# Kernel tuning notes

Hardware: AMD Instinct MI355X
Metric: run time of the kernel (lower is better)

The kernel has to match this reference:

```python
import jax, jax.numpy as jnp
import numpy as np

A, B, N = 8, 8, 2048


def setup_inputs() -> dict:
    key = jax.random.key(0)
    k1, k2 = jax.random.split(key)
    p_src = jax.random.normal(k1, (A, B, N, 2), dtype=jnp.float32)
    p_dst = jax.random.normal(k2, (A, B, N, 2), dtype=jnp.float32)
    return {"p_src": p_src, "p_dst": p_dst, "height": 480, "width": 640, "grid_scale": 1}


def reference(p_src, p_dst, height, width, grid_scale):
    a_dim, b_dim, n_pts = p_src.shape[:3]
    grid_h, grid_w = int(height * grid_scale), int(width * grid_scale)
    M = a_dim * b_dim * n_pts  # static upper bound on #matches

    # denormalize_pixel_coordinates(p, grid_h, grid_w): (x,y) -> ((p+1) * [(gw-1)/2, (gh-1)/2])
    scale = jnp.array([(grid_w - 1) / 2.0, (grid_h - 1) / 2.0], dtype=jnp.float32)
    coord_src = (p_src + 1.0) * scale  # [A,B,N,2] float grid coords (x,y)
    coord_dst = (p_dst + 1.0) * scale

    vis_src = jnp.all((p_src >= -1) & (p_src <= 1), axis=-1)  # [A,B,N]
    vis_dst = jnp.all((p_dst >= -1) & (p_dst <= 1), axis=-1)

    # integer cell coords; route invisible points out of bounds so scatter drops them
    xs = jnp.where(vis_src, coord_src[..., 0].astype(jnp.int32), grid_w).reshape(-1)
    ys = jnp.where(vis_src, coord_src[..., 1].astype(jnp.int32), grid_h).reshape(-1)
    xd = jnp.where(vis_dst, coord_dst[..., 0].astype(jnp.int32), grid_w).reshape(-1)
    yd = jnp.where(vis_dst, coord_dst[..., 1].astype(jnp.int32), grid_h).reshape(-1)

    ids = jnp.arange(M, dtype=jnp.int32)  # flat point index == torch's compacted-order rank
    aa = jnp.broadcast_to(jnp.arange(a_dim, dtype=jnp.int32)[:, None, None], (a_dim, b_dim, n_pts)).reshape(-1)
    bb = jnp.broadcast_to(jnp.arange(b_dim, dtype=jnp.int32)[None, :, None], (a_dim, b_dim, n_pts)).reshape(-1)

    grid0 = jnp.full((a_dim, b_dim, grid_w, grid_h), -1, dtype=jnp.int32)
    grid0 = grid0.at[aa, bb, xs, ys].max(ids, mode='drop')
    grid1 = jnp.full((a_dim, b_dim, grid_w, grid_h), -1, dtype=jnp.int32)
    grid1 = grid1.at[aa, bb, xd, yd].max(ids, mode='drop')

    mask_f = ((grid0 >= 0) & (grid1 >= 0)).reshape(-1)
    sel = jnp.nonzero(mask_f, size=M, fill_value=0)[0]  # row-major == torch boolean-mask order
    valid = jnp.arange(M) < jnp.sum(mask_f)

    src_idx = grid0.reshape(-1)[sel]  # flat point index of matched src point
    dst_idx = grid1.reshape(-1)[sel]

    # NOTE: faithful to source: factor pairs (height-1)/(grid_h-1) with the x column
    factor = jnp.array([(height - 1) / (grid_h - 1), (width - 1) / (grid_w - 1)], dtype=jnp.float32)
    csf = (coord_src * factor).reshape(-1, 2)
    cdf = (coord_dst * factor).reshape(-1, 2)

    src_coord_m = jnp.where(valid[:, None], csf[src_idx], 0.0)  # [M,2], padded with 0
    dst_coord_m = jnp.where(valid[:, None], cdf[dst_idx], 0.0)
    # visible_src_idx[:, match][[1,2]].T -> (b, n); visible_dst_idx[:, match][[0,2]].T -> (a, n)
    src_bn = jnp.where(valid[:, None], jnp.stack([(src_idx // n_pts) % b_dim, src_idx % n_pts], axis=-1), -1)
    dst_an = jnp.where(valid[:, None], jnp.stack([dst_idx // (b_dim * n_pts), dst_idx % n_pts], axis=-1), -1)
    return src_coord_m, dst_coord_m, src_bn, dst_an, valid
```

## Files before the change

### kernel.cpp

```cpp
#include <hip/hip_runtime.h>

#define AD 8
#define BD 8
#define NP 2048
#define MPTS (AD*BD*NP)
#define NIMG (AD*BD)
#define NSPI 4
#define NSEG (NIMG*NSPI)
#define HSZ 4096
#define RCAP 2048
#define DPAD 65536

__device__ int g_cnt[NSEG];
__device__ int g_rc[NSEG*RCAP];
__device__ int g_rs[NSEG*RCAP];
__device__ int g_rd[NSEG*RCAP];

__global__ __launch_bounds__(256) void k_hash(
    const float* __restrict__ ps, const float* __restrict__ pd,
    float* __restrict__ out,
    const int* __restrict__ ph, const int* __restrict__ pw,
    const int* __restrict__ pg) {
  __shared__ int hkey[HSZ];
  __shared__ int hsrc[HSZ];
  __shared__ int hdst[HSZ];
  __shared__ int lcnt;

  int b = blockIdx.x, tid = threadIdx.x;

  if (b >= NSEG) {
    const float4 z4  = make_float4(0.f, 0.f, 0.f, 0.f);
    const float4 m14 = make_float4(-1.f, -1.f, -1.f, -1.f);
    float4* o4 = (float4*)out;
    int pb = b - NSEG;
#pragma unroll
    for (int k = 0; k < 9; ++k) {
      int q4 = pb*2304 + k*256 + tid;
      if (q4 < 131072) {
        int arr = q4 >> 15, idx = q4 & 32767;
        o4[arr*(MPTS/2) + DPAD/2 + idx] = (arr < 2) ? z4 : m14;
      } else {
        o4[2*MPTS + DPAD/4 + (q4 - 131072)] = z4;
      }
    }
    return;
  }

  int img = b >> 2, seg = b & (NSPI - 1);

  for (int i = tid; i < HSZ; i += 256) { hkey[i] = -1; hsrc[i] = 0; hdst[i] = 0; }
  if (tid == 0) lcnt = 0;
  __syncthreads();

  int h = *ph, w = *pw, gs = *pg;
  int gh = h * gs, gw = w * gs;
  float sx = (float)((gw - 1) * 0.5);
  float sy = (float)((gh - 1) * 0.5);
  int ncell = gw * gh;
  int Q = (ncell + NSPI - 1) / NSPI;
  int clo = seg * Q;
  int chi = min(clo + Q, ncell);

  auto insert = [&](float px, float py, int gid, int* field) {
    if (!(px >= -1.f && px <= 1.f && py >= -1.f && py <= 1.f)) return;
    int c = (int)((px + 1.f) * sx) * gh + (int)((py + 1.f) * sy);
    if (c < clo || c >= chi) return;
    int i = (int)(((unsigned)c * 2654435761u) >> 20) & (HSZ - 1);
    while (true) {
      int k = atomicCAS(&hkey[i], -1, c);
      if (k == -1 || k == c) { atomicMax(&field[i], gid + 1); return; }
      i = (i + 1) & (HSZ - 1);
    }
  };

  const float4* sp = (const float4*)ps + img * (NP/2);
  const float4* dp = (const float4*)pd + img * (NP/2);
  int gbase = img * NP;
#pragma unroll
  for (int k = 0; k < NP/512; ++k) {
    int f = k*256 + tid;
    float4 s2 = sp[f];
    insert(s2.x, s2.y, gbase + 2*f,     hsrc);
    insert(s2.z, s2.w, gbase + 2*f + 1, hsrc);
    float4 d2 = dp[f];
    insert(d2.x, d2.y, gbase + 2*f,     hdst);
    insert(d2.z, d2.w, gbase + 2*f + 1, hdst);
  }
  __syncthreads();

  for (int i = tid; i < HSZ; i += 256) {
    if (hkey[i] >= 0) {
      int s = hsrc[i], d = hdst[i];
      if (s > 0 && d > 0) {
        int slot = atomicAdd(&lcnt, 1);
        g_rc[b*RCAP + slot] = hkey[i];
        g_rs[b*RCAP + slot] = s - 1;
        g_rd[b*RCAP + slot] = d - 1;
      }
    }
  }
  __syncthreads();
  if (tid == 0) g_cnt[b] = lcnt;
}

__global__ __launch_bounds__(256) void k_emit(
    const float* __restrict__ ps, const float* __restrict__ pd,
    float* __restrict__ out,
    const int* __restrict__ ph, const int* __restrict__ pw,
    const int* __restrict__ pg) {
  __shared__ int ssum[NSEG];
  int b = blockIdx.x, tid = threadIdx.x;
  int myc = g_cnt[tid];
  ssum[tid] = myc;
  for (int off = 1; off < NSEG; off <<= 1) {
    __syncthreads();
    int t = (tid >= off) ? ssum[tid - off] : 0;
    __syncthreads();
    ssum[tid] += t;
  }
  __syncthreads();

  int cnt = g_cnt[b];
  int soff = ssum[b] - cnt;
  int n = ssum[NSEG - 1];

  int h = *ph, w = *pw, gs = *pg;
  int gh = h * gs, gw = w * gs;
  float sx = (float)((gw - 1) * 0.5);
  float sy = (float)((gh - 1) * 0.5);
  float fxm = (float)((double)(h - 1) / (double)(gh - 1));
  float fym = (float)((double)(w - 1) / (double)(gw - 1));

  float* out0 = out;
  float* out1 = out + 2*MPTS;
  float* out2 = out + 4*MPTS;
  float* out3 = out + 6*MPTS;
  float* out4 = out + 8*MPTS;

  for (int j = tid; j < cnt; j += 256) {
    int ci = g_rc[b*RCAP + j];
    int rank = soff;
    for (int i = 0; i < cnt; ++i) rank += (int)(g_rc[b*RCAP + i] < ci);
    int s = g_rs[b*RCAP + j], d = g_rd[b*RCAP + j];
    float2 a2 = ((const float2*)ps)[s];
    out0[2*rank]   = (a2.x + 1.f) * sx * fxm;
    out0[2*rank+1] = (a2.y + 1.f) * sy * fym;
    float2 b2 = ((const float2*)pd)[d];
    out1[2*rank]   = (b2.x + 1.f) * sx * fxm;
    out1[2*rank+1] = (b2.y + 1.f) * sy * fym;
    out2[2*rank]   = (float)((s / NP) % BD);
    out2[2*rank+1] = (float)(s % NP);
    out3[2*rank]   = (float)(d / (BD * NP));
    out3[2*rank+1] = (float)(d % NP);
    out4[rank]     = 1.f;
  }

  int rr = n + b*256 + tid;
  if (rr < MPTS) {
    float2* o2 = (float2*)out;
    o2[rr]          = make_float2(0.f, 0.f);
    o2[MPTS + rr]   = make_float2(0.f, 0.f);
    o2[2*MPTS + rr] = make_float2(-1.f, -1.f);
    o2[3*MPTS + rr] = make_float2(-1.f, -1.f);
    out[8*MPTS + rr] = 0.f;
  }
}

extern "C" void kernel_launch(void* const* d_in, const int* in_sizes, int n_in,
                              void* d_out, int out_size, void* d_ws, size_t ws_size,
                              hipStream_t stream) {
  const float* ps = (const float*)d_in[0];
  const float* pd = (const float*)d_in[1];
  const int* ph = (const int*)d_in[2];
  const int* pw = (const int*)d_in[3];
  const int* pg = (const int*)d_in[4];
  float* out = (float*)d_out;

  k_hash<<<NSEG + 64, 256, 0, stream>>>(ps, pd, out, ph, pw, pg);
  k_emit<<<NSEG,      256, 0, stream>>>(ps, pd, out, ph, pw, pg);
}
```

Before: 16.86 us.

## Split each image into eight cell segments and scan counts with wave shuffles

Result: faster. 16.17 us (-4.1%).

```diff
diff --git a/kernel.cpp b/kernel.cpp
--- a/kernel.cpp
+++ b/kernel.cpp
@@ -5,11 +5,10 @@
 #define NP 2048
 #define MPTS (AD*BD*NP)
 #define NIMG (AD*BD)
-#define NSPI 4
+#define NSPI 8
 #define NSEG (NIMG*NSPI)
 #define HSZ 4096
 #define RCAP 2048
-#define DPAD 65536
 
 __device__ int g_cnt[NSEG];
 __device__ int g_rc[NSEG*RCAP];
@@ -18,7 +17,6 @@
 
 __global__ __launch_bounds__(256) void k_hash(
     const float* __restrict__ ps, const float* __restrict__ pd,
-    float* __restrict__ out,
     const int* __restrict__ ph, const int* __restrict__ pw,
     const int* __restrict__ pg) {
   __shared__ int hkey[HSZ];
@@ -27,26 +25,7 @@
   __shared__ int lcnt;
 
   int b = blockIdx.x, tid = threadIdx.x;
-
-  if (b >= NSEG) {
-    const float4 z4  = make_float4(0.f, 0.f, 0.f, 0.f);
-    const float4 m14 = make_float4(-1.f, -1.f, -1.f, -1.f);
-    float4* o4 = (float4*)out;
-    int pb = b - NSEG;
-#pragma unroll
-    for (int k = 0; k < 9; ++k) {
-      int q4 = pb*2304 + k*256 + tid;
-      if (q4 < 131072) {
-        int arr = q4 >> 15, idx = q4 & 32767;
-        o4[arr*(MPTS/2) + DPAD/2 + idx] = (arr < 2) ? z4 : m14;
-      } else {
-        o4[2*MPTS + DPAD/4 + (q4 - 131072)] = z4;
-      }
-    }
-    return;
-  }
-
-  int img = b >> 2, seg = b & (NSPI - 1);
+  int img = b >> 3, seg = b & (NSPI - 1);
 
   for (int i = tid; i < HSZ; i += 256) { hkey[i] = -1; hsrc[i] = 0; hdst[i] = 0; }
   if (tid == 0) lcnt = 0;
@@ -103,26 +82,38 @@
   if (tid == 0) g_cnt[b] = lcnt;
 }
 
-__global__ __launch_bounds__(256) void k_emit(
+__global__ __launch_bounds__(512) void k_emit(
     const float* __restrict__ ps, const float* __restrict__ pd,
     float* __restrict__ out,
     const int* __restrict__ ph, const int* __restrict__ pw,
     const int* __restrict__ pg) {
   __shared__ int ssum[NSEG];
+  __shared__ int wsum[8];
   int b = blockIdx.x, tid = threadIdx.x;
-  int myc = g_cnt[tid];
-  ssum[tid] = myc;
-  for (int off = 1; off < NSEG; off <<= 1) {
-    __syncthreads();
-    int t = (tid >= off) ? ssum[tid - off] : 0;
-    __syncthreads();
-    ssum[tid] += t;
+  int lane = tid & 63, wv = tid >> 6;
+
+  int x = g_cnt[tid];
+  for (int off = 1; off < 64; off <<= 1) {
+    int t = __shfl_up(x, off, 64);
+    if (lane >= off) x += t;
+  }
+  if (lane == 63) wsum[wv] = x;
+  __syncthreads();
+  if (tid < 8) {
+    int t = wsum[tid];
+    for (int off = 1; off < 8; off <<= 1) {
+      int u = __shfl_up(t, off, 8);
+      if (tid >= off) t += u;
+    }
+    wsum[tid] = t;
   }
   __syncthreads();
+  ssum[tid] = x + (wv ? wsum[wv - 1] : 0);
+  __syncthreads();
 
-  int cnt = g_cnt[b];
-  int soff = ssum[b] - cnt;
-  int n = ssum[NSEG - 1];
+  int soff = b ? ssum[b - 1] : 0;
+  int cnt  = ssum[b] - soff;
+  int n    = ssum[NSEG - 1];
 
   int h = *ph, w = *pw, gs = *pg;
   int gh = h * gs, gw = w * gs;
@@ -137,7 +128,7 @@
   float* out3 = out + 6*MPTS;
   float* out4 = out + 8*MPTS;
 
-  for (int j = tid; j < cnt; j += 256) {
+  for (int j = tid; j < cnt; j += 512) {
     int ci = g_rc[b*RCAP + j];
     int rank = soff;
     for (int i = 0; i < cnt; ++i) rank += (int)(g_rc[b*RCAP + i] < ci);
@@ -155,7 +146,7 @@
     out4[rank]     = 1.f;
   }
 
-  int rr = n + b*256 + tid;
+  int rr = n + b*512 + tid;
   if (rr < MPTS) {
     float2* o2 = (float2*)out;
     o2[rr]          = make_float2(0.f, 0.f);
@@ -176,6 +167,6 @@
   const int* pg = (const int*)d_in[4];
   float* out = (float*)d_out;
 
-  k_hash<<<NSEG + 64, 256, 0, stream>>>(ps, pd, out, ph, pw, pg);
-  k_emit<<<NSEG,      256, 0, stream>>>(ps, pd, out, ph, pw, pg);
+  k_hash<<<NSEG, 256, 0, stream>>>(ps, pd, ph, pw, pg);
+  k_emit<<<NSEG, 512, 0, stream>>>(ps, pd, out, ph, pw, pg);
 }
```
